# Optimization experiments

Hardware: AMD Instinct MI355X
Metric: run time of the kernel (lower is better)

The kernel has to match this reference:

```python
import jax, jax.numpy as jnp
import numpy as np

NQ, NK = 32, 128          # block height / width (AF3 local attention)
INF = 1.0e9
EPS = 1e-5


def _ln(x, w=None, b=None):
    m = jnp.mean(x, axis=-1, keepdims=True)
    v = jnp.var(x, axis=-1, keepdims=True)
    y = (x - m) * jax.lax.rsqrt(v + EPS)
    if w is not None:
        y = y * w
    if b is not None:
        y = y + b
    return y


def _key_idx(N):
    # For query block i, keys cover a window of NK atoms centered on the block.
    nb = N // NQ
    start = np.arange(nb)[:, None] * NQ - (NK - NQ) // 2
    idx = start + np.arange(NK)[None, :]          # [nb, NK]
    valid = ((idx >= 0) & (idx < N)).astype(np.float32)
    return np.clip(idx, 0, N - 1), valid


def setup_inputs() -> dict:
    key = jax.random.key(0)
    ks = iter(jax.random.split(key, 32))
    B, N, C, CZ, H, CH, CS = 4, 8192, 128, 16, 4, 32, 128
    nb = N // NQ
    nrm = lambda sh, sc=0.02: jax.random.normal(next(ks), sh, jnp.float32) * sc
    return dict(
        a=nrm((B, N, C), 1.0),
        z=nrm((B, nb, NQ, NK, CZ), 1.0),
        s=nrm((B, N, CS), 1.0),
        mask=jnp.ones((B, N), jnp.float32),
        ln_s_q_w=jnp.ones((CS,), jnp.float32),
        Wg_q=nrm((CS, C)), bg_q=jnp.zeros((C,), jnp.float32), Wb_q=nrm((CS, C)),
        ln_s_k_w=jnp.ones((CS,), jnp.float32),
        Wg_k=nrm((CS, C)), bg_k=jnp.zeros((C,), jnp.float32), Wb_k=nrm((CS, C)),
        ln_z_w=jnp.ones((CZ,), jnp.float32), ln_z_b=jnp.zeros((CZ,), jnp.float32),
        W_z=nrm((CZ, H)),
        Wq=nrm((C, H * CH)), Wk=nrm((C, H * CH)), Wv=nrm((C, H * CH)),
        Wg=nrm((C, H * CH)), bg=jnp.ones((H * CH,), jnp.float32),
        Wo=nrm((H * CH, C)), bo=jnp.zeros((C,), jnp.float32),
        W_ado=nrm((CS, C)), b_ado=jnp.full((C,), -2.0, jnp.float32),
    )


def reference(a, z, s, mask,
              ln_s_q_w, Wg_q, bg_q, Wb_q,
              ln_s_k_w, Wg_k, bg_k, Wb_k,
              ln_z_w, ln_z_b, W_z,
              Wq, Wk, Wv, Wg, bg, Wo, bo,
              W_ado, b_ado):
    B, N, C = a.shape
    H = W_z.shape[1]
    CH = Wq.shape[1] // H
    nb = N // NQ
    idx, valid = _key_idx(N)

    # --- block inputs ---
    a_q = a.reshape(B, nb, NQ, C)            # [B, nb, NQ, C]
    a_k = a[:, idx]                          # [B, nb, NK, C]
    q_mask = mask.reshape(B, nb, NQ)
    k_mask = mask[:, idx] * valid            # [B, nb, NK]
    pair_mask = q_mask[..., :, None] * k_mask[..., None, :]   # [B, nb, NQ, NK]
    mask_bias = (INF * (pair_mask - 1.0))[..., None, :, :]     # [B, nb, 1, NQ, NK]

    # --- pair bias from z ---
    zb = _ln(z, ln_z_w, ln_z_b) @ W_z        # [B, nb, NQ, NK, H]
    zb = jnp.moveaxis(zb, -1, -3)            # [B, nb, H, NQ, NK]

    # --- AdaLN conditioning ---
    s_q = s.reshape(B, nb, NQ, -1)
    s_k = s[:, idx]
    sqn = _ln(s_q, ln_s_q_w)
    skn = _ln(s_k, ln_s_k_w)
    aq = jax.nn.sigmoid(sqn @ Wg_q + bg_q) * _ln(a_q) + sqn @ Wb_q
    ak = jax.nn.sigmoid(skn @ Wg_k + bg_k) * _ln(a_k) + skn @ Wb_k

    # --- blocked attention with pair bias ---
    scale = 1.0 / np.sqrt(CH).astype(np.float32)
    q = (aq @ Wq).reshape(B, nb, NQ, H, CH) * scale
    k = (ak @ Wk).reshape(B, nb, NK, H, CH)
    v = (ak @ Wv).reshape(B, nb, NK, H, CH)
    logits = jnp.einsum('bnqhc,bnkhc->bnhqk', q, k) + mask_bias + zb
    attn = jax.nn.softmax(logits, axis=-1)
    o = jnp.einsum('bnhqk,bnkhc->bnqhc', attn, v)
    g = jax.nn.sigmoid(aq @ Wg + bg).reshape(B, nb, NQ, H, CH)
    o = (g * o).reshape(B, nb, NQ, H * CH)
    out = (o @ Wo + bo).reshape(B, N, C)[:, :N, :]

    # --- AdaLN-Zero output gate ---
    out = jax.nn.sigmoid(s @ W_ado + b_ado) * out
    return out
```

## Files before the change

kernel.cpp:

```cpp
#include <hip/hip_runtime.h>
#include <cstdint>
#include <cstddef>

#define B_ 4
#define N_ 8192
#define C_ 128
#define NB_ 256
#define EPS_ 1e-5f

typedef unsigned int u32;
typedef unsigned short u16;

typedef short bf16x8 __attribute__((ext_vector_type(8)));
typedef float f32x4 __attribute__((ext_vector_type(4)));
union U16x8 { uint4 u4; bf16x8 v; };

__device__ __forceinline__ float bf2f(u16 v){ union{u32 i; float f;} x; x.i = ((u32)v)<<16; return x.f; }
__device__ __forceinline__ u16 f2bf(float f){ union{float f; u32 i;} x; x.f=f; u32 r = x.i + 0x7fffu + ((x.i>>16)&1u); return (u16)(r>>16); }
__device__ __forceinline__ u32 pk2(float a, float b){ return (u32)f2bf(a) | ((u32)f2bf(b)<<16); }
__device__ __forceinline__ float sigm(float x){ return 1.f/(1.f+__expf(-x)); }

__global__ void k0_prep(const float* __restrict__ Wgq, const float* __restrict__ Wbq,
                        const float* __restrict__ Wgk, const float* __restrict__ Wbk,
                        const float* __restrict__ Wado, const float* __restrict__ Wq_,
                        const float* __restrict__ Wg_, const float* __restrict__ Wk_,
                        const float* __restrict__ Wv_, const float* __restrict__ Wo_,
                        const float* __restrict__ lnsqw, const float* __restrict__ lnskw,
                        const float* __restrict__ lnzw, const float* __restrict__ lnzb,
                        const float* __restrict__ Wz,
                        const float* __restrict__ gz, const float* __restrict__ gmask,
                        u16* __restrict__ PW, float* __restrict__ AUX, u16* __restrict__ ZB)
{
  __shared__ float WZL[72];
  if (blockIdx.x < 81) {
    if (blockIdx.x < 80) {
      int gid = blockIdx.x*256 + threadIdx.x;
      int mat = gid >> 11;
      int rem = gid & 2047;
      int ks = rem >> 9;
      int rem2 = rem & 511;
      int nt = rem2 >> 6;
      int lane = rem2 & 63;
      int kbase = ks*32 + (lane>>4)*8;
      int n = nt*16 + (lane&15);
      const float* W; int scmode = 0; float fixed = 1.f;
      switch (mat) {
        case 0: W = Wgq; scmode = 1; break;
        case 1: W = Wbq; scmode = 1; break;
        case 2: W = Wgk; scmode = 2; break;
        case 3: W = Wbk; scmode = 2; break;
        case 4: W = Wado; break;
        case 5: W = Wq_; fixed = 0.17677669529663687f; break;
        case 6: W = Wg_; break;
        case 7: W = Wk_; break;
        case 8: W = Wv_; break;
        default: W = Wo_; break;
      }
      u16 o[8];
      #pragma unroll
      for (int j=0;j<8;j++){
        int k = kbase + j;
        float sc = fixed;
        if (scmode == 1) sc *= lnsqw[k];
        else if (scmode == 2) sc *= lnskw[k];
        o[j] = f2bf(W[k*128 + n] * sc);
      }
      uint4 pk;
      pk.x = (u32)o[0] | ((u32)o[1]<<16); pk.y = (u32)o[2] | ((u32)o[3]<<16);
      pk.z = (u32)o[4] | ((u32)o[5]<<16); pk.w = (u32)o[6] | ((u32)o[7]<<16);
      *(uint4*)(PW + (size_t)gid*8) = pk;
    } else {
      int t = threadIdx.x;
      if (t < 128) {
        float s = 0.f;
        for (int k=0;k<128;k++) s += Wado[k*128 + t];
        AUX[t] = s;
      }
    }
    return;
  }

  {
    int t = (int)threadIdx.x;
    if (t < 64) WZL[t] = lnzw[t>>2] * Wz[t];
    else if (t < 68) { int h = t-64; float s=0.f; for (int c=0;c<16;c++) s += lnzw[c]*Wz[c*4+h]; WZL[64+h]=s; }
    else if (t < 72) { int h = t-68; float s=0.f; for (int c=0;c<16;c++) s += lnzb[c]*Wz[c*4+h]; WZL[68+h]=s; }
  }
  __syncthreads();

  const int blk = (int)blockIdx.x - 81;
  const int bi = blk >> 3;
  const int kg = blk & 7;
  const int b = bi >> 8, i = bi & 255;
  const int t = (int)threadIdx.x;
  const int q = t & 31, kl = t >> 5;
  const int key0 = kg*16 + kl, key1 = key0 + 8;

  const float* z0 = gz + (size_t)bi*65536 + ((size_t)q*128 + key0)*16;
  const float* z1 = z0 + 8*16;
  float4 a0 = *(const float4*)(z0);      float4 a1 = *(const float4*)(z0+4);
  float4 a2 = *(const float4*)(z0+8);    float4 a3 = *(const float4*)(z0+12);
  float4 c0 = *(const float4*)(z1);      float4 c1 = *(const float4*)(z1+4);
  float4 c2 = *(const float4*)(z1+8);    float4 c3 = *(const float4*)(z1+12);

  const float qm = gmask[(size_t)b*N_ + i*32 + q];
  int raw0 = i*32 - 48 + key0;
  int raw1 = i*32 - 48 + key1;
  float km0 = (raw0 >= 0 && raw0 < N_) ? gmask[(size_t)b*N_ + raw0] : 0.f;
  float km1 = (raw1 >= 0 && raw1 < N_) ? gmask[(size_t)b*N_ + raw1] : 0.f;
  float mb0 = 1000000000.0f*(qm*km0 - 1.f);
  float mb1 = 1000000000.0f*(qm*km1 - 1.f);

  u16* zbase = ZB + (size_t)bi*16384 + q;
  #pragma unroll
  for (int p=0;p<2;p++){
    float zv[16];
    if (p==0){ zv[0]=a0.x;zv[1]=a0.y;zv[2]=a0.z;zv[3]=a0.w; zv[4]=a1.x;zv[5]=a1.y;zv[6]=a1.z;zv[7]=a1.w;
               zv[8]=a2.x;zv[9]=a2.y;zv[10]=a2.z;zv[11]=a2.w; zv[12]=a3.x;zv[13]=a3.y;zv[14]=a3.z;zv[15]=a3.w; }
    else     { zv[0]=c0.x;zv[1]=c0.y;zv[2]=c0.z;zv[3]=c0.w; zv[4]=c1.x;zv[5]=c1.y;zv[6]=c1.z;zv[7]=c1.w;
               zv[8]=c2.x;zv[9]=c2.y;zv[10]=c2.z;zv[11]=c2.w; zv[12]=c3.x;zv[13]=c3.y;zv[14]=c3.z;zv[15]=c3.w; }
    float sm=0.f, sq=0.f, S0=0.f, S1=0.f, S2=0.f, S3=0.f;
    #pragma unroll
    for (int c=0;c<16;c++){
      sm += zv[c]; sq = fmaf(zv[c],zv[c],sq);
      S0 = fmaf(zv[c], WZL[c*4+0], S0); S1 = fmaf(zv[c], WZL[c*4+1], S1);
      S2 = fmaf(zv[c], WZL[c*4+2], S2); S3 = fmaf(zv[c], WZL[c*4+3], S3);
    }
    float mz = sm*(1.f/16.f);
    float rz = rsqrtf(sq*(1.f/16.f) - mz*mz + EPS_);
    float mb = p ? mb1 : mb0;
    int key = p ? key1 : key0;
    u16* zo = zbase + key*32;
    zo[0*4096] = f2bf((S0 - mz*WZL[64])*rz + WZL[68] + mb);
    zo[1*4096] = f2bf((S1 - mz*WZL[65])*rz + WZL[69] + mb);
    zo[2*4096] = f2bf((S2 - mz*WZL[66])*rz + WZL[70] + mb);
    zo[3*4096] = f2bf((S3 - mz*WZL[67])*rz + WZL[71] + mb);
  }
}

__device__ __forceinline__ void mm_single(f32x4 acc[4][2], const u16* Abase, const u16* __restrict__ PW,
                                          int mat, int wave, int lane, int lq, int quad)
{
  #pragma unroll
  for (int ks=0; ks<4; ks++){
    U16x8 b0, b1;
    b0.u4 = *(const uint4*)(PW + (size_t)((((mat*4+ks)*8) + wave*2+0)*64 + lane)*8);
    b1.u4 = *(const uint4*)(PW + (size_t)((((mat*4+ks)*8) + wave*2+1)*64 + lane)*8);
    #pragma unroll
    for (int mt=0; mt<4; mt++){
      U16x8 a; a.u4 = *(const uint4*)(Abase + (mt*16+lq)*136 + ks*32 + quad*8);
      acc[mt][0] = __builtin_amdgcn_mfma_f32_16x16x32_bf16(a.v, b0.v, acc[mt][0], 0,0,0);
      acc[mt][1] = __builtin_amdgcn_mfma_f32_16x16x32_bf16(a.v, b1.v, acc[mt][1], 0,0,0);
    }
  }
}
__device__ __forceinline__ void mm_dual(f32x4 acc1[4][2], int m1, f32x4 acc2[4][2], int m2,
                                        const u16* Abase, const u16* __restrict__ PW,
                                        int wave, int lane, int lq, int quad)
{
  #pragma unroll
  for (int ks=0; ks<4; ks++){
    U16x8 b10, b11, b20, b21;
    b10.u4 = *(const uint4*)(PW + (size_t)((((m1*4+ks)*8) + wave*2+0)*64 + lane)*8);
    b11.u4 = *(const uint4*)(PW + (size_t)((((m1*4+ks)*8) + wave*2+1)*64 + lane)*8);
    b20.u4 = *(const uint4*)(PW + (size_t)((((m2*4+ks)*8) + wave*2+0)*64 + lane)*8);
    b21.u4 = *(const uint4*)(PW + (size_t)((((m2*4+ks)*8) + wave*2+1)*64 + lane)*8);
    #pragma unroll
    for (int mt=0; mt<4; mt++){
      U16x8 a; a.u4 = *(const uint4*)(Abase + (mt*16+lq)*136 + ks*32 + quad*8);
      acc1[mt][0] = __builtin_amdgcn_mfma_f32_16x16x32_bf16(a.v, b10.v, acc1[mt][0], 0,0,0);
      acc1[mt][1] = __builtin_amdgcn_mfma_f32_16x16x32_bf16(a.v, b11.v, acc1[mt][1], 0,0,0);
      acc2[mt][0] = __builtin_amdgcn_mfma_f32_16x16x32_bf16(a.v, b20.v, acc2[mt][0], 0,0,0);
      acc2[mt][1] = __builtin_amdgcn_mfma_f32_16x16x32_bf16(a.v, b21.v, acc2[mt][1], 0,0,0);
    }
  }
}
#define ZERO82(A) do{ _Pragma("unroll") for(int _m=0;_m<4;_m++){ A[_m][0]=(f32x4)(0.f); A[_m][1]=(f32x4)(0.f);} }while(0)

__global__ __launch_bounds__(256, 2)
void k1_proj(const float* __restrict__ ga, const float* __restrict__ gs,
             const float* __restrict__ bgq, const float* __restrict__ bgk,
             const float* __restrict__ bg, const float* __restrict__ bado,
             const u16* __restrict__ PW, const float* __restrict__ AUX,
             u16* __restrict__ Q, u16* __restrict__ K, u16* __restrict__ VT,
             u16* __restrict__ G, u16* __restrict__ ADO)
{
  __shared__ char arena[52736];
  u16* SN  = (u16*)arena;
  u16* LNA = (u16*)(arena + 17408);
  u16* AQ  = (u16*)(arena + 34816);
  float* SSTAT = (float*)(arena + 52224);

  const int tid = (int)threadIdx.x;
  const int rowbase = (int)blockIdx.x * 64;
  const int b = rowbase >> 13;
  const int nb0 = rowbase & 8191;
  const int wave = tid >> 6, lane = tid & 63;
  const int lq = lane & 15, quad = lane >> 4;

  {
    const float* sbase = gs + (size_t)rowbase*128;
    const float* abase = ga + (size_t)rowbase*128;
    #pragma unroll 1
    for (int t=0;t<8;t++){
      int chunk = t*256 + tid;
      int row = chunk >> 5;
      int k4 = (chunk & 31) * 4;
      float4 vs = *(const float4*)(sbase + (size_t)chunk*4);
      float4 va = *(const float4*)(abase + (size_t)chunk*4);
      float sm = vs.x+vs.y+vs.z+vs.w, sq = vs.x*vs.x+vs.y*vs.y+vs.z*vs.z+vs.w*vs.w;
      float am = va.x+va.y+va.z+va.w, a2 = va.x*va.x+va.y*va.y+va.z*va.z+va.w*va.w;
      #pragma unroll
      for (int m=1;m<32;m<<=1){
        sm += __shfl_xor(sm,m,32); sq += __shfl_xor(sq,m,32);
        am += __shfl_xor(am,m,32); a2 += __shfl_xor(a2,m,32);
      }
      float smean = sm*(1.f/128.f);
      float svar  = sq*(1.f/128.f) - smean*smean;
      float srstd = rsqrtf(svar + EPS_);
      float amean = am*(1.f/128.f);
      float avar  = a2*(1.f/128.f) - amean*amean;
      float arstd = rsqrtf(avar + EPS_);
      *(uint2*)(SN + row*136 + k4) = make_uint2(
        pk2((vs.x-smean)*srstd,(vs.y-smean)*srstd), pk2((vs.z-smean)*srstd,(vs.w-smean)*srstd));
      *(uint2*)(LNA + row*136 + k4) = make_uint2(
        pk2((va.x-amean)*arstd,(va.y-amean)*arstd), pk2((va.z-amean)*arstd,(va.w-amean)*arstd));
      if ((tid & 31) == 0){
        SSTAT[row*2]   = smean;
        SSTAT[row*2+1] = (svar + EPS_)*srstd;
      }
    }
  }
  __syncthreads();

  const int cg0 = wave*32 + lq;
  const int cg1 = cg0 + 16;

  {
    f32x4 acc[4][2]; ZERO82(acc);
    mm_single(acc, SN, PW, 4, wave, lane, lq, quad);
    float cs0 = AUX[cg0], cs1 = AUX[cg1];
    float bb0 = bado[cg0], bb1 = bado[cg1];
    #pragma unroll
    for (int mt=0; mt<4; mt++){
      #pragma unroll
      for (int reg=0; reg<4; reg++){
        int row = mt*16 + quad*4 + reg;
        float mean = SSTAT[row*2], std = SSTAT[row*2+1];
        ADO[(size_t)(rowbase+row)*128 + cg0] = f2bf(sigm(std*acc[mt][0][reg] + mean*cs0 + bb0));
        ADO[(size_t)(rowbase+row)*128 + cg1] = f2bf(sigm(std*acc[mt][1][reg] + mean*cs1 + bb1));
      }
    }
  }

  {
    f32x4 aG[4][2], aB[4][2]; ZERO82(aG); ZERO82(aB);
    mm_dual(aG, 0, aB, 1, SN, PW, wave, lane, lq, quad);
    float bq0 = bgq[cg0], bq1 = bgq[cg1];
    #pragma unroll
    for (int mt=0; mt<4; mt++){
      #pragma unroll
      for (int reg=0; reg<4; reg++){
        int row = mt*16 + quad*4 + reg;
        float l0 = bf2f(LNA[row*136 + cg0]), l1 = bf2f(LNA[row*136 + cg1]);
        AQ[row*136 + cg0] = f2bf(sigm(aG[mt][0][reg]+bq0)*l0 + aB[mt][0][reg]);
        AQ[row*136 + cg1] = f2bf(sigm(aG[mt][1][reg]+bq1)*l1 + aB[mt][1][reg]);
      }
    }
  }

  {
    f32x4 aG[4][2], aB[4][2]; ZERO82(aG); ZERO82(aB);
    mm_dual(aG, 2, aB, 3, SN, PW, wave, lane, lq, quad);
    float bk0 = bgk[cg0], bk1 = bgk[cg1];
    #pragma unroll
    for (int mt=0; mt<4; mt++){
      #pragma unroll
      for (int reg=0; reg<4; reg++){
        int row = mt*16 + quad*4 + reg;
        float l0 = bf2f(LNA[row*136 + cg0]), l1 = bf2f(LNA[row*136 + cg1]);
        aG[mt][0][reg] = sigm(aG[mt][0][reg]+bk0)*l0 + aB[mt][0][reg];
        aG[mt][1][reg] = sigm(aG[mt][1][reg]+bk1)*l1 + aB[mt][1][reg];
      }
    }
    __syncthreads();
    #pragma unroll
    for (int mt=0; mt<4; mt++){
      #pragma unroll
      for (int reg=0; reg<4; reg++){
        int row = mt*16 + quad*4 + reg;
        SN[row*136 + cg0] = f2bf(aG[mt][0][reg]);
        SN[row*136 + cg1] = f2bf(aG[mt][1][reg]);
      }
    }
    __syncthreads();
  }

  {
    f32x4 aQ_[4][2], aG_[4][2]; ZERO82(aQ_); ZERO82(aG_);
    mm_dual(aQ_, 5, aG_, 6, AQ, PW, wave, lane, lq, quad);
    float bg0 = bg[cg0], bg1 = bg[cg1];
    #pragma unroll
    for (int mt=0; mt<4; mt++){
      #pragma unroll
      for (int reg=0; reg<4; reg++){
        int row = mt*16 + quad*4 + reg;
        Q[(size_t)(rowbase+row)*128 + cg0] = f2bf(aQ_[mt][0][reg]);
        Q[(size_t)(rowbase+row)*128 + cg1] = f2bf(aQ_[mt][1][reg]);
        G[(size_t)(rowbase+row)*128 + cg0] = f2bf(sigm(aG_[mt][0][reg]+bg0));
        G[(size_t)(rowbase+row)*128 + cg1] = f2bf(sigm(aG_[mt][1][reg]+bg1));
      }
    }
  }

  {
    f32x4 aK_[4][2], aV_[4][2]; ZERO82(aK_); ZERO82(aV_);
    mm_dual(aK_, 7, aV_, 8, SN, PW, wave, lane, lq, quad);
    #pragma unroll
    for (int mt=0; mt<4; mt++){
      #pragma unroll
      for (int reg=0; reg<4; reg++){
        int row = mt*16 + quad*4 + reg;
        K[(size_t)(rowbase+row)*128 + cg0] = f2bf(aK_[mt][0][reg]);
        K[(size_t)(rowbase+row)*128 + cg1] = f2bf(aK_[mt][1][reg]);
      }
      ushort4 p0, p1;
      p0.x = f2bf(aV_[mt][0][0]); p0.y = f2bf(aV_[mt][0][1]);
      p0.z = f2bf(aV_[mt][0][2]); p0.w = f2bf(aV_[mt][0][3]);
      p1.x = f2bf(aV_[mt][1][0]); p1.y = f2bf(aV_[mt][1][1]);
      p1.z = f2bf(aV_[mt][1][2]); p1.w = f2bf(aV_[mt][1][3]);
      int nloc = nb0 + mt*16 + quad*4;
      *(ushort4*)(VT + ((size_t)(b*128 + cg0))*N_ + nloc) = p0;
      *(ushort4*)(VT + ((size_t)(b*128 + cg1))*N_ + nloc) = p1;
    }
  }
}

__global__ __launch_bounds__(256, 4)
void k2_attn(const float* __restrict__ bo,
             const u16* __restrict__ PW,
             const u16* __restrict__ Q, const u16* __restrict__ K,
             const u16* __restrict__ VT, const u16* __restrict__ G,
             const u16* __restrict__ ADO, const u16* __restrict__ ZB,
             float* __restrict__ gout)
{
  __shared__ char arena[34816];
  u16* ATTall = (u16*)arena;
  u16* GO     = (u16*)arena;

  const int flat = (int)blockIdx.x;
  const int x = flat & 7, r = flat >> 3;
  const int j = r & 31, b = r >> 5;
  const int i = x*32 + j;

  const int tid = (int)threadIdx.x;
  const int wave = tid >> 6, lane = tid & 63;
  const int lq = lane & 15, quad = lane >> 4;
  const int h = wave;
  const int start = i*32 - 48;
  u16* ATT = ATTall + h*(32*136);

  f32x4 L[2][8];
  #pragma unroll
  for (int mt=0;mt<2;mt++) for (int nt=0;nt<8;nt++) L[mt][nt] = (f32x4)(0.f);
  {
    U16x8 aQ[2];
    #pragma unroll
    for (int mt=0;mt<2;mt++)
      aQ[mt].u4 = *(const uint4*)(Q + ((size_t)b*N_ + i*32 + mt*16 + lq)*128 + h*32 + quad*8);
    #pragma unroll
    for (int nt=0;nt<8;nt++){
      int kr = min(max(start + nt*16 + lq, 0), N_-1);
      U16x8 bk; bk.u4 = *(const uint4*)(K + ((size_t)b*N_ + kr)*128 + h*32 + quad*8);
      L[0][nt] = __builtin_amdgcn_mfma_f32_16x16x32_bf16(aQ[0].v, bk.v, L[0][nt], 0,0,0);
      L[1][nt] = __builtin_amdgcn_mfma_f32_16x16x32_bf16(aQ[1].v, bk.v, L[1][nt], 0,0,0);
    }
  }

  {
    const u16* zbb = ZB + (size_t)(b*NB_ + i)*16384 + h*4096;
    #pragma unroll
    for (int nt=0;nt<8;nt++){
      #pragma unroll
      for (int mt=0;mt<2;mt++){
        ushort4 z4 = *(const ushort4*)(zbb + (nt*16+lq)*32 + mt*16 + quad*4);
        L[mt][nt][0] += bf2f(z4.x); L[mt][nt][1] += bf2f(z4.y);
        L[mt][nt][2] += bf2f(z4.z); L[mt][nt][3] += bf2f(z4.w);
      }
    }
  }

  #pragma unroll
  for (int mt=0;mt<2;mt++){
    #pragma unroll
    for (int reg=0;reg<4;reg++){
      float mx = -3.0e38f;
      #pragma unroll
      for (int nt=0;nt<8;nt++) mx = fmaxf(mx, L[mt][nt][reg]);
      mx = fmaxf(mx, __shfl_xor(mx,1,16));
      mx = fmaxf(mx, __shfl_xor(mx,2,16));
      mx = fmaxf(mx, __shfl_xor(mx,4,16));
      mx = fmaxf(mx, __shfl_xor(mx,8,16));
      float e[8]; float s = 0.f;
      #pragma unroll
      for (int nt=0;nt<8;nt++){ e[nt] = __expf(L[mt][nt][reg]-mx); s += e[nt]; }
      s += __shfl_xor(s,1,16);
      s += __shfl_xor(s,2,16);
      s += __shfl_xor(s,4,16);
      s += __shfl_xor(s,8,16);
      float inv = 1.f/s;
      int q = mt*16 + quad*4 + reg;
      #pragma unroll
      for (int nt=0;nt<8;nt++) ATT[q*136 + nt*16 + lq] = f2bf(e[nt]*inv);
    }
  }

  f32x4 O[2][2];
  O[0][0]=(f32x4)(0.f); O[0][1]=(f32x4)(0.f); O[1][0]=(f32x4)(0.f); O[1][1]=(f32x4)(0.f);
  #pragma unroll
  for (int ks=0;ks<4;ks++){
    U16x8 ba[2];
    #pragma unroll
    for (int nt=0;nt<2;nt++)
      ba[nt].u4 = *(const uint4*)(ATT + (nt*16+lq)*136 + ks*32 + quad*8);
    int kk = start + ks*32 + quad*8;
    kk = min(max(kk,0), N_-8);
    #pragma unroll
    for (int mt=0;mt<2;mt++){
      U16x8 av;
      av.u4 = *(const uint4*)(VT + ((size_t)(b*128 + h*32 + mt*16 + lq))*N_ + kk);
      O[mt][0] = __builtin_amdgcn_mfma_f32_16x16x32_bf16(av.v, ba[0].v, O[mt][0], 0,0,0);
      O[mt][1] = __builtin_amdgcn_mfma_f32_16x16x32_bf16(av.v, ba[1].v, O[mt][1], 0,0,0);
    }
  }
  __syncthreads();

  #pragma unroll
  for (int mt=0;mt<2;mt++){
    #pragma unroll
    for (int nt=0;nt<2;nt++){
      int q = nt*16 + lq;
      int cb = h*32 + mt*16 + quad*4;
      ushort4 g4 = *(const ushort4*)(G + ((size_t)b*N_ + i*32 + q)*128 + cb);
      ushort4 p;
      p.x = f2bf(bf2f(g4.x)*O[mt][nt][0]); p.y = f2bf(bf2f(g4.y)*O[mt][nt][1]);
      p.z = f2bf(bf2f(g4.z)*O[mt][nt][2]); p.w = f2bf(bf2f(g4.w)*O[mt][nt][3]);
      *(ushort4*)(GO + q*136 + cb) = p;
    }
  }
  __syncthreads();

  {
    f32x4 U[2][2];
    U[0][0]=(f32x4)(0.f); U[0][1]=(f32x4)(0.f); U[1][0]=(f32x4)(0.f); U[1][1]=(f32x4)(0.f);
    #pragma unroll
    for (int ks=0;ks<4;ks++){
      U16x8 b0, b1;
      b0.u4 = *(const uint4*)(PW + (size_t)((((9*4+ks)*8) + wave*2+0)*64 + lane)*8);
      b1.u4 = *(const uint4*)(PW + (size_t)((((9*4+ks)*8) + wave*2+1)*64 + lane)*8);
      #pragma unroll
      for (int mt=0;mt<2;mt++){
        U16x8 a; a.u4 = *(const uint4*)(GO + (mt*16+lq)*136 + ks*32 + quad*8);
        U[mt][0] = __builtin_amdgcn_mfma_f32_16x16x32_bf16(a.v, b0.v, U[mt][0], 0,0,0);
        U[mt][1] = __builtin_amdgcn_mfma_f32_16x16x32_bf16(a.v, b1.v, U[mt][1], 0,0,0);
      }
    }
    const int cg0 = wave*32 + lq, cg1 = cg0 + 16;
    float b00 = bo[cg0], b01 = bo[cg1];
    #pragma unroll
    for (int mt=0;mt<2;mt++){
      #pragma unroll
      for (int reg=0;reg<4;reg++){
        int q = mt*16 + quad*4 + reg;
        size_t rowoff = ((size_t)b*N_ + i*32 + q)*128;
        float ad0 = bf2f(ADO[rowoff + cg0]);
        float ad1 = bf2f(ADO[rowoff + cg1]);
        gout[rowoff + cg0] = ad0*(U[mt][0][reg] + b00);
        gout[rowoff + cg1] = ad1*(U[mt][1][reg] + b01);
      }
    }
  }
}

extern "C" void kernel_launch(void* const* d_in, const int* in_sizes, int n_in,
                              void* d_out, int out_size, void* d_ws, size_t ws_size,
                              hipStream_t stream) {
  (void)in_sizes; (void)n_in; (void)out_size; (void)ws_size;
  const float* ga    = (const float*)d_in[0];
  const float* gz    = (const float*)d_in[1];
  const float* gs    = (const float*)d_in[2];
  const float* gmask = (const float*)d_in[3];
  const float* lnsqw = (const float*)d_in[4];
  const float* Wgq   = (const float*)d_in[5];
  const float* bgq   = (const float*)d_in[6];
  const float* Wbq   = (const float*)d_in[7];
  const float* lnskw = (const float*)d_in[8];
  const float* Wgk   = (const float*)d_in[9];
  const float* bgk   = (const float*)d_in[10];
  const float* Wbk   = (const float*)d_in[11];
  const float* lnzw  = (const float*)d_in[12];
  const float* lnzb  = (const float*)d_in[13];
  const float* Wz    = (const float*)d_in[14];
  const float* Wq    = (const float*)d_in[15];
  const float* Wk    = (const float*)d_in[16];
  const float* Wv    = (const float*)d_in[17];
  const float* Wg    = (const float*)d_in[18];
  const float* bg    = (const float*)d_in[19];
  const float* Wo    = (const float*)d_in[20];
  const float* bo    = (const float*)d_in[21];
  const float* Wado  = (const float*)d_in[22];
  const float* bado  = (const float*)d_in[23];

  char* ws = (char*)d_ws;
  u16* Qb  = (u16*)(ws + 0);
  u16* Kb  = (u16*)(ws + 8388608);
  u16* VTb = (u16*)(ws + 16777216);
  u16* Gb  = (u16*)(ws + 25165824);
  u16* ADOb= (u16*)(ws + 33554432);
  u16* ZBb = (u16*)(ws + 41943040);
  u16* PW  = (u16*)(ws + 75497472);
  float* AUX = (float*)(ws + 75497472 + 327680);

  k0_prep<<<81 + 8192, 256, 0, stream>>>(Wgq, Wbq, Wgk, Wbk, Wado, Wq, Wg, Wk, Wv, Wo,
                                         lnsqw, lnskw, lnzw, lnzb, Wz, gz, gmask,
                                         PW, AUX, ZBb);
  k1_proj<<<512, 256, 0, stream>>>(ga, gs, bgq, bgk, bg, bado, PW, AUX,
                                   Qb, Kb, VTb, Gb, ADOb);
  k2_attn<<<1024, 256, 0, stream>>>(bo, PW, Qb, Kb, VTb, Gb, ADOb, ZBb, (float*)d_out);
}
```

Before: 463.7 us.

## Merge pair-bias computation into projection kernel with interleaved block roles

Moves the z layernorm/pair-bias computation out of the prep kernel and into the projection kernel. Block indices are interleaved so two of every three blocks compute pair bias and the third runs the projection path. The pair-bias work is restaged through shared memory so each block handles a whole query block and writes ZB with coalesced 16-byte stores instead of scattered 2-byte stores. The aim is to overlap the memory-bound z read with the MFMA-heavy projection and to improve write coalescing. The cost is larger shared-memory use for the z-only blocks and an extra synchronisation.

```diff
diff --git a/kernel.cpp b/kernel.cpp
--- a/kernel.cpp
+++ b/kernel.cpp
@@ -26,115 +26,51 @@
                         const float* __restrict__ Wg_, const float* __restrict__ Wk_,
                         const float* __restrict__ Wv_, const float* __restrict__ Wo_,
                         const float* __restrict__ lnsqw, const float* __restrict__ lnskw,
-                        const float* __restrict__ lnzw, const float* __restrict__ lnzb,
-                        const float* __restrict__ Wz,
-                        const float* __restrict__ gz, const float* __restrict__ gmask,
-                        u16* __restrict__ PW, float* __restrict__ AUX, u16* __restrict__ ZB)
+                        u16* __restrict__ PW, float* __restrict__ AUX)
 {
-  __shared__ float WZL[72];
-  if (blockIdx.x < 81) {
-    if (blockIdx.x < 80) {
-      int gid = blockIdx.x*256 + threadIdx.x;
-      int mat = gid >> 11;
-      int rem = gid & 2047;
-      int ks = rem >> 9;
-      int rem2 = rem & 511;
-      int nt = rem2 >> 6;
-      int lane = rem2 & 63;
-      int kbase = ks*32 + (lane>>4)*8;
-      int n = nt*16 + (lane&15);
-      const float* W; int scmode = 0; float fixed = 1.f;
-      switch (mat) {
-        case 0: W = Wgq; scmode = 1; break;
-        case 1: W = Wbq; scmode = 1; break;
-        case 2: W = Wgk; scmode = 2; break;
-        case 3: W = Wbk; scmode = 2; break;
-        case 4: W = Wado; break;
-        case 5: W = Wq_; fixed = 0.17677669529663687f; break;
-        case 6: W = Wg_; break;
-        case 7: W = Wk_; break;
-        case 8: W = Wv_; break;
-        default: W = Wo_; break;
-      }
-      u16 o[8];
-      #pragma unroll
-      for (int j=0;j<8;j++){
-        int k = kbase + j;
-        float sc = fixed;
-        if (scmode == 1) sc *= lnsqw[k];
-        else if (scmode == 2) sc *= lnskw[k];
-        o[j] = f2bf(W[k*128 + n] * sc);
-      }
-      uint4 pk;
-      pk.x = (u32)o[0] | ((u32)o[1]<<16); pk.y = (u32)o[2] | ((u32)o[3]<<16);
-      pk.z = (u32)o[4] | ((u32)o[5]<<16); pk.w = (u32)o[6] | ((u32)o[7]<<16);
-      *(uint4*)(PW + (size_t)gid*8) = pk;
-    } else {
-      int t = threadIdx.x;
-      if (t < 128) {
-        float s = 0.f;
-        for (int k=0;k<128;k++) s += Wado[k*128 + t];
-        AUX[t] = s;
-      }
-    }
-    return;
-  }
-
-  {
-    int t = (int)threadIdx.x;
-    if (t < 64) WZL[t] = lnzw[t>>2] * Wz[t];
-    else if (t < 68) { int h = t-64; float s=0.f; for (int c=0;c<16;c++) s += lnzw[c]*Wz[c*4+h]; WZL[64+h]=s; }
-    else if (t < 72) { int h = t-68; float s=0.f; for (int c=0;c<16;c++) s += lnzb[c]*Wz[c*4+h]; WZL[68+h]=s; }
-  }
-  __syncthreads();
-
-  const int blk = (int)blockIdx.x - 81;
-  const int bi = blk >> 3;
-  const int kg = blk & 7;
-  const int b = bi >> 8, i = bi & 255;
-  const int t = (int)threadIdx.x;
-  const int q = t & 31, kl = t >> 5;
-  const int key0 = kg*16 + kl, key1 = key0 + 8;
-
-  const float* z0 = gz + (size_t)bi*65536 + ((size_t)q*128 + key0)*16;
-  const float* z1 = z0 + 8*16;
-  float4 a0 = *(const float4*)(z0);      float4 a1 = *(const float4*)(z0+4);
-  float4 a2 = *(const float4*)(z0+8);    float4 a3 = *(const float4*)(z0+12);
-  float4 c0 = *(const float4*)(z1);      float4 c1 = *(const float4*)(z1+4);
-  float4 c2 = *(const float4*)(z1+8);    float4 c3 = *(const float4*)(z1+12);
-
-  const float qm = gmask[(size_t)b*N_ + i*32 + q];
-  int raw0 = i*32 - 48 + key0;
-  int raw1 = i*32 - 48 + key1;
-  float km0 = (raw0 >= 0 && raw0 < N_) ? gmask[(size_t)b*N_ + raw0] : 0.f;
-  float km1 = (raw1 >= 0 && raw1 < N_) ? gmask[(size_t)b*N_ + raw1] : 0.f;
-  float mb0 = 1000000000.0f*(qm*km0 - 1.f);
-  float mb1 = 1000000000.0f*(qm*km1 - 1.f);
-
-  u16* zbase = ZB + (size_t)bi*16384 + q;
-  #pragma unroll
-  for (int p=0;p<2;p++){
-    float zv[16];
-    if (p==0){ zv[0]=a0.x;zv[1]=a0.y;zv[2]=a0.z;zv[3]=a0.w; zv[4]=a1.x;zv[5]=a1.y;zv[6]=a1.z;zv[7]=a1.w;
-               zv[8]=a2.x;zv[9]=a2.y;zv[10]=a2.z;zv[11]=a2.w; zv[12]=a3.x;zv[13]=a3.y;zv[14]=a3.z;zv[15]=a3.w; }
-    else     { zv[0]=c0.x;zv[1]=c0.y;zv[2]=c0.z;zv[3]=c0.w; zv[4]=c1.x;zv[5]=c1.y;zv[6]=c1.z;zv[7]=c1.w;
-               zv[8]=c2.x;zv[9]=c2.y;zv[10]=c2.z;zv[11]=c2.w; zv[12]=c3.x;zv[13]=c3.y;zv[14]=c3.z;zv[15]=c3.w; }
-    float sm=0.f, sq=0.f, S0=0.f, S1=0.f, S2=0.f, S3=0.f;
-    #pragma unroll
-    for (int c=0;c<16;c++){
-      sm += zv[c]; sq = fmaf(zv[c],zv[c],sq);
-      S0 = fmaf(zv[c], WZL[c*4+0], S0); S1 = fmaf(zv[c], WZL[c*4+1], S1);
-      S2 = fmaf(zv[c], WZL[c*4+2], S2); S3 = fmaf(zv[c], WZL[c*4+3], S3);
-    }
-    float mz = sm*(1.f/16.f);
-    float rz = rsqrtf(sq*(1.f/16.f) - mz*mz + EPS_);
-    float mb = p ? mb1 : mb0;
-    int key = p ? key1 : key0;
-    u16* zo = zbase + key*32;
-    zo[0*4096] = f2bf((S0 - mz*WZL[64])*rz + WZL[68] + mb);
-    zo[1*4096] = f2bf((S1 - mz*WZL[65])*rz + WZL[69] + mb);
-    zo[2*4096] = f2bf((S2 - mz*WZL[66])*rz + WZL[70] + mb);
-    zo[3*4096] = f2bf((S3 - mz*WZL[67])*rz + WZL[71] + mb);
+  if (blockIdx.x < 80) {
+    int gid = blockIdx.x*256 + threadIdx.x;
+    int mat = gid >> 11;
+    int rem = gid & 2047;
+    int ks = rem >> 9;
+    int rem2 = rem & 511;
+    int nt = rem2 >> 6;
+    int lane = rem2 & 63;
+    int kbase = ks*32 + (lane>>4)*8;
+    int n = nt*16 + (lane&15);
+    const float* W; int scmode = 0; float fixed = 1.f;
+    switch (mat) {
+      case 0: W = Wgq; scmode = 1; break;
+      case 1: W = Wbq; scmode = 1; break;
+      case 2: W = Wgk; scmode = 2; break;
+      case 3: W = Wbk; scmode = 2; break;
+      case 4: W = Wado; break;
+      case 5: W = Wq_; fixed = 0.17677669529663687f; break;
+      case 6: W = Wg_; break;
+      case 7: W = Wk_; break;
+      case 8: W = Wv_; break;
+      default: W = Wo_; break;
+    }
+    u16 o[8];
+    #pragma unroll
+    for (int j=0;j<8;j++){
+      int k = kbase + j;
+      float sc = fixed;
+      if (scmode == 1) sc *= lnsqw[k];
+      else if (scmode == 2) sc *= lnskw[k];
+      o[j] = f2bf(W[k*128 + n] * sc);
+    }
+    uint4 pk;
+    pk.x = (u32)o[0] | ((u32)o[1]<<16); pk.y = (u32)o[2] | ((u32)o[3]<<16);
+    pk.z = (u32)o[4] | ((u32)o[5]<<16); pk.w = (u32)o[6] | ((u32)o[7]<<16);
+    *(uint4*)(PW + (size_t)gid*8) = pk;
+  } else {
+    int t = threadIdx.x;
+    if (t < 128) {
+      float s = 0.f;
+      for (int k=0;k<128;k++) s += Wado[k*128 + t];
+      AUX[t] = s;
+    }
   }
 }
 
@@ -178,21 +114,92 @@
 #define ZERO82(A) do{ _Pragma("unroll") for(int _m=0;_m<4;_m++){ A[_m][0]=(f32x4)(0.f); A[_m][1]=(f32x4)(0.f);} }while(0)
 
 __global__ __launch_bounds__(256, 2)
-void k1_proj(const float* __restrict__ ga, const float* __restrict__ gs,
-             const float* __restrict__ bgq, const float* __restrict__ bgk,
-             const float* __restrict__ bg, const float* __restrict__ bado,
-             const u16* __restrict__ PW, const float* __restrict__ AUX,
-             u16* __restrict__ Q, u16* __restrict__ K, u16* __restrict__ VT,
-             u16* __restrict__ G, u16* __restrict__ ADO)
+void kf_fused(const float* __restrict__ ga, const float* __restrict__ gs,
+              const float* __restrict__ gz, const float* __restrict__ gmask,
+              const float* __restrict__ lnzw, const float* __restrict__ lnzb,
+              const float* __restrict__ Wz,
+              const float* __restrict__ bgq, const float* __restrict__ bgk,
+              const float* __restrict__ bg, const float* __restrict__ bado,
+              const u16* __restrict__ PW, const float* __restrict__ AUX,
+              u16* __restrict__ Q, u16* __restrict__ K, u16* __restrict__ VT,
+              u16* __restrict__ G, u16* __restrict__ ADO, u16* __restrict__ ZB)
 {
   __shared__ char arena[52736];
+  const int blk = (int)blockIdx.x;
+  const int mod = blk % 3;
+  const int tid = (int)threadIdx.x;
+
+  if (mod != 2) {
+    u16* ZT   = (u16*)arena;
+    float* WZL = (float*)(arena + 36864);
+    float* QMV = (float*)(arena + 37152);
+    float* KMV = (float*)(arena + 37280);
+    const int bi = (blk/3)*2 + mod;
+    const int b = bi >> 8, i = bi & 255;
+
+    if (tid < 64) WZL[tid] = lnzw[tid>>2] * Wz[tid];
+    else if (tid < 68) { int h = tid-64; float s=0.f; for (int c=0;c<16;c++) s += lnzw[c]*Wz[c*4+h]; WZL[64+h]=s; }
+    else if (tid < 72) { int h = tid-68; float s=0.f; for (int c=0;c<16;c++) s += lnzb[c]*Wz[c*4+h]; WZL[68+h]=s; }
+    else if (tid >= 96 && tid < 128) QMV[tid-96] = gmask[(size_t)b*N_ + i*32 + (tid-96)];
+    else if (tid >= 128) {
+      int k = tid - 128;
+      int raw = i*32 - 48 + k;
+      KMV[k] = (raw >= 0 && raw < N_) ? gmask[(size_t)b*N_ + raw] : 0.f;
+    }
+    __syncthreads();
+
+    #pragma unroll 1
+    for (int it=0; it<16; ++it){
+      int g = it*256 + tid;
+      const float* zp = gz + (size_t)bi*65536 + (size_t)g*16;
+      float4 z0 = *(const float4*)(zp);
+      float4 z1 = *(const float4*)(zp+4);
+      float4 z2 = *(const float4*)(zp+8);
+      float4 z3 = *(const float4*)(zp+12);
+      int q = g >> 7, key = g & 127;
+      float zv[16] = {z0.x,z0.y,z0.z,z0.w, z1.x,z1.y,z1.z,z1.w,
+                      z2.x,z2.y,z2.z,z2.w, z3.x,z3.y,z3.z,z3.w};
+      float sm=0.f, sq=0.f, S0=0.f, S1=0.f, S2=0.f, S3=0.f;
+      #pragma unroll
+      for (int c=0;c<16;c++){
+        sm += zv[c]; sq = fmaf(zv[c],zv[c],sq);
+        S0 = fmaf(zv[c], WZL[c*4+0], S0); S1 = fmaf(zv[c], WZL[c*4+1], S1);
+        S2 = fmaf(zv[c], WZL[c*4+2], S2); S3 = fmaf(zv[c], WZL[c*4+3], S3);
+      }
+      float mz = sm*(1.f/16.f);
+      float rz = rsqrtf(sq*(1.f/16.f) - mz*mz + EPS_);
+      float mb = 1000000000.0f*(QMV[q]*KMV[key] - 1.f);
+      int base = key*36 + q;
+      ZT[0*4608 + base] = f2bf((S0 - mz*WZL[64])*rz + WZL[68] + mb);
+      ZT[1*4608 + base] = f2bf((S1 - mz*WZL[65])*rz + WZL[69] + mb);
+      ZT[2*4608 + base] = f2bf((S2 - mz*WZL[66])*rz + WZL[70] + mb);
+      ZT[3*4608 + base] = f2bf((S3 - mz*WZL[67])*rz + WZL[71] + mb);
+    }
+    __syncthreads();
+
+    u16* dst = ZB + (size_t)bi*16384;
+    const int key = tid >> 1, q0 = (tid & 1)*16;
+    #pragma unroll
+    for (int h=0; h<4; h++){
+      const u16* src = ZT + h*4608 + key*36 + q0;
+      uint2 w0 = *(const uint2*)(src);
+      uint2 w1 = *(const uint2*)(src+4);
+      uint2 w2 = *(const uint2*)(src+8);
+      uint2 w3 = *(const uint2*)(src+12);
+      uint4 o0; o0.x=w0.x; o0.y=w0.y; o0.z=w1.x; o0.w=w1.y;
+      uint4 o1; o1.x=w2.x; o1.y=w2.y; o1.z=w3.x; o1.w=w3.y;
+      *(uint4*)(dst + h*4096 + tid*16)     = o0;
+      *(uint4*)(dst + h*4096 + tid*16 + 8) = o1;
+    }
+    return;
+  }
+
   u16* SN  = (u16*)arena;
   u16* LNA = (u16*)(arena + 17408);
   u16* AQ  = (u16*)(arena + 34816);
   float* SSTAT = (float*)(arena + 52224);
 
-  const int tid = (int)threadIdx.x;
-  const int rowbase = (int)blockIdx.x * 64;
+  const int rowbase = (blk/3) * 64;
   const int b = rowbase >> 13;
   const int nb0 = rowbase & 8191;
   const int wave = tid >> 6, lane = tid & 63;
@@ -521,10 +528,10 @@
   u16* PW  = (u16*)(ws + 75497472);
   float* AUX = (float*)(ws + 75497472 + 327680);
 
-  k0_prep<<<81 + 8192, 256, 0, stream>>>(Wgq, Wbq, Wgk, Wbk, Wado, Wq, Wg, Wk, Wv, Wo,
-                                         lnsqw, lnskw, lnzw, lnzb, Wz, gz, gmask,
-                                         PW, AUX, ZBb);
-  k1_proj<<<512, 256, 0, stream>>>(ga, gs, bgq, bgk, bg, bado, PW, AUX,
-                                   Qb, Kb, VTb, Gb, ADOb);
+  k0_prep<<<81, 256, 0, stream>>>(Wgq, Wbq, Wgk, Wbk, Wado, Wq, Wg, Wk, Wv, Wo,
+                                  lnsqw, lnskw, PW, AUX);
+  kf_fused<<<1536, 256, 0, stream>>>(ga, gs, gz, gmask, lnzw, lnzb, Wz,
+                                     bgq, bgk, bg, bado, PW, AUX,
+                                     Qb, Kb, VTb, Gb, ADOb, ZBb);
   k2_attn<<<1024, 256, 0, stream>>>(bo, PW, Qb, Kb, VTb, Gb, ADOb, ZBb, (float*)d_out);
 }
```

Result: no change. 470.2 us (+1.4%).
